# Kernel tuning notes

Measured on AMD Instinct MI355X. Metric: run time of the kernel, lower is better.

Reference implementation:

```python
import jax, jax.numpy as jnp
import numpy as np

N_NODES = 50000
N_EDGES = 600000
D = 128
EPS = 1e-5
AVG_D_LOG = float(np.log(4 + 1))  # avg_d={'log': log(avg_d+1)}, avg_d=4


def setup_inputs() -> dict:
    key = jax.random.key(0)
    ks = jax.random.split(key, 8)
    h = jax.random.normal(ks[0], (N_NODES, D), dtype=jnp.float32)
    # guarantee every node has at least one incoming edge (self-loop)
    edge_dst = jnp.concatenate([
        jnp.arange(N_NODES, dtype=jnp.int64),
        jax.random.randint(ks[1], (N_EDGES - N_NODES,), 0, N_NODES).astype(jnp.int64),
    ])
    edge_src = jax.random.randint(ks[2], (N_EDGES,), 0, N_NODES).astype(jnp.int64)
    def lin(k, fan_in, fan_out):
        lim = 1.0 / np.sqrt(fan_in)
        return jax.random.uniform(k, (fan_in, fan_out), jnp.float32, -lim, lim)
    W_pre = lin(ks[3], 2 * D, D)
    b_pre = jnp.zeros((D,), jnp.float32)
    W_post = lin(ks[4], 12 * D + D, D)  # 4 aggregators * 3 scalers * D + in_dim
    b_post = jnp.zeros((D,), jnp.float32)
    W_mix = lin(ks[5], D, D)
    b_mix = jnp.zeros((D,), jnp.float32)
    return {"h": h, "edge_src": edge_src, "edge_dst": edge_dst,
            "W_pre": W_pre, "b_pre": b_pre, "W_post": W_post,
            "b_post": b_post, "W_mix": W_mix, "b_mix": b_mix}


def reference(h, edge_src, edge_dst, W_pre, b_pre, W_post, b_post, W_mix, b_mix):
    n = h.shape[0]
    # pretrans_edges: cat(src, dst) -> Linear -> ReLU (MLP act) -> ReLU (outer)
    z2 = jnp.concatenate([h[edge_src], h[edge_dst]], axis=1)        # [E, 2D]
    e = jax.nn.relu(z2 @ W_pre + b_pre)                             # [E, D]
    # multi-aggregator segment reduce over destination nodes
    deg = jax.ops.segment_sum(jnp.ones_like(edge_dst, jnp.float32), edge_dst, n)  # [N]
    inv_deg = 1.0 / deg[:, None]
    mean = jax.ops.segment_sum(e, edge_dst, n) * inv_deg
    mean_sq = jax.ops.segment_sum(e * e, edge_dst, n) * inv_deg
    std = jnp.sqrt(jax.nn.relu(mean_sq - mean * mean) + EPS)
    mx = jax.ops.segment_max(e, edge_dst, n)
    mn = jax.ops.segment_min(e, edge_dst, n)
    agg = jnp.concatenate([mean, mx, mn, std], axis=1)              # [N, 4D]
    # scalers: identity, amplification, attenuation
    log_d = jnp.log(deg + 1.0)[:, None]
    scaled = jnp.concatenate([agg, agg * (log_d / AVG_D_LOG), agg * (AVG_D_LOG / log_d)], axis=1)  # [N, 12D]
    # posttrans: cat(h, aggregated) -> Linear -> ReLU
    hp = jax.nn.relu(jnp.concatenate([h, scaled], axis=1) @ W_post + b_post)  # [N, D]
    # mixing network + residual (node_dim == out_dim)
    out = h + jax.nn.leaky_relu(hp @ W_mix + b_mix, negative_slope=0.01)
    return out
```

## Files before the change

### kernel.cpp

```cpp
#include <hip/hip_runtime.h>
#include <hip/hip_bf16.h>

#define N_NODES 50000
#define N_EDGES 600000
#define D 128

constexpr float AVG_D_LOG = 1.6094379124341003f;
constexpr float EPS_V = 1e-5f;

#define PQ_B     0ul
#define AGG_B    25600000ul
#define HBF_B    76800000ul
#define WPRET2_B 89600000ul
#define WPOSTT_B 89665536ul
#define WMIXT_B  90091520ul
#define DEGC_B   90124288ul
#define OFF_B    90324288ul
#define CUR_B    90524352ul
#define SRCS_B   90724352ul
#define GCNT_B   93124352ul

typedef __attribute__((ext_vector_type(8))) short bf16x8;
typedef __attribute__((ext_vector_type(4))) float f32x4;

__device__ __forceinline__ short f2b(float f) {
    unsigned u = __builtin_bit_cast(unsigned, f);
    u += 0x7fffu + ((u >> 16) & 1u);
    return (short)(u >> 16);
}
__device__ __forceinline__ unsigned pk2(float a, float b) {
    return (unsigned)(unsigned short)f2b(a) | ((unsigned)(unsigned short)f2b(b) << 16);
}
__device__ __forceinline__ float blo(unsigned u) { return __uint_as_float(u << 16); }
__device__ __forceinline__ float bhi(unsigned u) { return __uint_as_float(u & 0xffff0000u); }

__device__ __forceinline__ void gld_lds16(const void* g, void* l) {
    __builtin_amdgcn_global_load_lds(
        (const __attribute__((address_space(1))) void*)g,
        (__attribute__((address_space(3))) void*)l, 16, 0, 0);
}

#define WAIT_BAR(N) do {                                              \
    asm volatile("s_waitcnt vmcnt(" #N ")" ::: "memory");             \
    __builtin_amdgcn_sched_barrier(0);                                \
    __builtin_amdgcn_s_barrier();                                     \
    __builtin_amdgcn_sched_barrier(0);                                \
} while (0)
#define BAR_ONLY() do {                                               \
    __builtin_amdgcn_sched_barrier(0);                                \
    __builtin_amdgcn_s_barrier();                                     \
    __builtin_amdgcn_sched_barrier(0);                                \
} while (0)
#define SB0() __builtin_amdgcn_sched_barrier(0)

__global__ __launch_bounds__(256) void prep_kernel(
    const float* __restrict__ h, const float* __restrict__ Wpre,
    const float* __restrict__ Wpost, const float* __restrict__ Wmix,
    short* __restrict__ hbf, short* __restrict__ wpreT2,
    short* __restrict__ wpostT, short* __restrict__ wmixT,
    int* __restrict__ degc, int* __restrict__ cursor, int* __restrict__ gcnt)
{
    long i = (long)blockIdx.x * 256 + threadIdx.x;
    if (i < 800000) {
        float4 a = *(const float4*)(h + i * 8);
        float4 b = *(const float4*)(h + i * 8 + 4);
        int4 v;
        v.x = (int)pk2(a.x, a.y); v.y = (int)pk2(a.z, a.w);
        v.z = (int)pk2(b.x, b.y); v.w = (int)pk2(b.z, b.w);
        *(int4*)(hbf + i * 8) = v;
        return;
    }
    i -= 800000;
    if (i < 32768) {
        int n = i >> 7, k = i & 127;
        float v = (n < 128) ? Wpre[k * 128 + n] : Wpre[(k + 128) * 128 + (n - 128)];
        wpreT2[n * 128 + k] = f2b(v);
        return;
    }
    i -= 32768;
    if (i < 212992) { int k = i >> 7, n = i & 127; wpostT[n * 1664 + k] = f2b(Wpost[k * 128 + n]); return; }
    i -= 212992;
    if (i < 16384) { int k = i >> 7, n = i & 127; wmixT[n * 128 + k] = f2b(Wmix[k * 128 + n]); return; }
    i -= 16384;
    if (i < N_NODES) { degc[i] = 0; return; }
    i -= N_NODES;
    if (i < N_NODES) { cursor[i] = 0; return; }
    i -= N_NODES;
    if (i == 0) *gcnt = 0;
}
#define PREP_BLOCKS ((800000 + 32768 + 212992 + 16384 + 2 * N_NODES + 1 + 255) / 256)

__global__ __launch_bounds__(256) void hist_kernel(const int* __restrict__ edst, int* __restrict__ degc) {
    int e = blockIdx.x * 256 + threadIdx.x;
    if (e < N_EDGES) atomicAdd(&degc[edst[e]], 1);
}

__global__ __launch_bounds__(256) void alloc_kernel(const int* __restrict__ degc,
                                                    int* __restrict__ off, int* __restrict__ gcnt) {
    int n = blockIdx.x * 256 + threadIdx.x;
    int d = (n < N_NODES) ? degc[n] : 0;
    int pre = d;
#pragma unroll
    for (int o = 1; o < 64; o <<= 1) {
        int t = __shfl_up(pre, o);
        if ((threadIdx.x & 63) >= o) pre += t;
    }
    int base = 0;
    if ((threadIdx.x & 63) == 63) base = atomicAdd(gcnt, pre);
    base = __shfl(base, 63);
    if (n < N_NODES) off[n] = base + pre - d;
}

__global__ __launch_bounds__(256) void scatter_kernel(const int* __restrict__ esrc, const int* __restrict__ edst,
                                                      const int* __restrict__ off, int* __restrict__ cursor,
                                                      int* __restrict__ srcs) {
    int e = blockIdx.x * 256 + threadIdx.x;
    if (e < N_EDGES) {
        int d = edst[e];
        int p = off[d] + atomicAdd(&cursor[d], 1);
        srcs[p] = esrc[e];
    }
}

__device__ __forceinline__ void stageA_t(short* ldsT, const short* src, int rs, int co,
                                         int bn, int wv, int lane) {
    const int sub = lane >> 3, seg = lane & 7;
    const int sg = (seg ^ sub) * 8;
#pragma unroll
    for (int t = 0; t < 4; t++) {
        int i = wv * 4 + t;
        int row = i * 8 + sub;
        int n = bn + row; if (n >= N_NODES) n = N_NODES - 1;
        gld_lds16(src + (long)n * rs + co + sg, ldsT + i * 512);
    }
}
__device__ __forceinline__ void stageB_t(short* ldsT, const short* src, int rs, int co,
                                         int wv, int lane) {
    const int sub = lane >> 3, seg = lane & 7;
    const int sg = (seg ^ sub) * 8;
#pragma unroll
    for (int t = 0; t < 4; t++) {
        int i = wv * 4 + t;
        int row = i * 8 + sub;
        gld_lds16(src + (long)row * rs + co + sg, ldsT + i * 512);
    }
}
__device__ __forceinline__ void loadAfr(bf16x8* a, const short* src, int rs, int co,
                                        int bn, int wv, int lm, int quad) {
#pragma unroll
    for (int rt = 0; rt < 2; rt++)
#pragma unroll
        for (int ks = 0; ks < 2; ks++) {
            int n = bn + wv * 32 + rt * 16 + lm; if (n >= N_NODES) n = N_NODES - 1;
            a[rt * 2 + ks] = *(const bf16x8*)(src + (long)n * rs + co + ks * 32 + quad * 8);
        }
}

#define MFMA_ITER(AB, BB, ACC)                                                      \
    {                                                                               \
        _Pragma("unroll")                                                           \
        for (int ks = 0; ks < 2; ks++) {                                            \
            const int qx = (((ks * 4 + quad) ^ r7) * 8);                            \
            bf16x8 a0 = *(const bf16x8*)&(AB)[(wv * 32 + lm) * 64 + qx];            \
            bf16x8 a1 = *(const bf16x8*)&(AB)[(wv * 32 + 16 + lm) * 64 + qx];       \
            _Pragma("unroll")                                                       \
            for (int ct = 0; ct < 8; ct++) {                                        \
                bf16x8 b = *(const bf16x8*)&(BB)[(ct * 16 + lm) * 64 + qx];         \
                ACC[0][ct] = __builtin_amdgcn_mfma_f32_16x16x32_bf16(b, a0, ACC[0][ct], 0, 0, 0); \
                ACC[1][ct] = __builtin_amdgcn_mfma_f32_16x16x32_bf16(b, a1, ACC[1][ct], 0, 0, 0); \
            }                                                                       \
        }                                                                           \
    }

#define MFMA_RG(BB, AF, ACC, FRESH)                                                 \
    {                                                                               \
        __builtin_amdgcn_s_setprio(1);                                              \
        _Pragma("unroll")                                                           \
        for (int ks = 0; ks < 2; ks++) {                                            \
            const int qx = ((ks * 4 + quad) ^ r7) * 8;                              \
            _Pragma("unroll")                                                       \
            for (int ct = 0; ct < 8; ct++) {                                        \
                bf16x8 b = *(const bf16x8*)&(BB)[(ct * 16 + lm) * 64 + qx];         \
                f32x4 c0 = ((FRESH) && ks == 0) ? (f32x4){0.f, 0.f, 0.f, 0.f} : ACC[0][ct]; \
                f32x4 c1 = ((FRESH) && ks == 0) ? (f32x4){0.f, 0.f, 0.f, 0.f} : ACC[1][ct]; \
                ACC[0][ct] = __builtin_amdgcn_mfma_f32_16x16x32_bf16(b, (AF)[ks], c0, 0, 0, 0); \
                ACC[1][ct] = __builtin_amdgcn_mfma_f32_16x16x32_bf16(b, (AF)[2 + ks], c1, 0, 0, 0); \
            }                                                                       \
        }                                                                           \
        __builtin_amdgcn_s_setprio(0);                                              \
    }

__global__ __launch_bounds__(256, 2) void gemm_pq_kernel(
    const short* __restrict__ hbf, const short* __restrict__ wpreT2,
    const float* __restrict__ bpre, short* __restrict__ PQ)
{
    __shared__ __align__(16) short As[2][8192];
    __shared__ __align__(16) short Bs[2][8192];

    const int tid = threadIdx.x;
    const int cg = blockIdx.x & 1;
    const int bn = (blockIdx.x >> 1) * 128;
    const int lane = tid & 63, wv = tid >> 6;
    const int lm = lane & 15, quad = lane >> 4;
    const int r7 = lm & 7;
    const short* Bsrc = wpreT2 + cg * 128 * 128;

    f32x4 acc[2][8];
#pragma unroll
    for (int a = 0; a < 2; a++)
#pragma unroll
        for (int b = 0; b < 8; b++) acc[a][b] = (f32x4){0.f, 0.f, 0.f, 0.f};

    stageA_t(As[0], hbf, 128, 0, bn, wv, lane);
    stageB_t(Bs[0], Bsrc, 128, 0, wv, lane);
    stageA_t(As[1], hbf, 128, 64, bn, wv, lane);
    stageB_t(Bs[1], Bsrc, 128, 64, wv, lane);
    WAIT_BAR(8);
    MFMA_ITER(As[0], Bs[0], acc);
    WAIT_BAR(0);
    MFMA_ITER(As[1], Bs[1], acc);

#pragma unroll
    for (int rt = 0; rt < 2; rt++) {
        int row = wv * 32 + rt * 16 + lm;
        int n = bn + row;
        if (n >= N_NODES) continue;
        short* dst = PQ + (long)n * 256;
#pragma unroll
        for (int ct = 0; ct < 8; ct++) {
            int col = cg * 128 + ct * 16 + quad * 4;
            float v0 = acc[rt][ct][0], v1 = acc[rt][ct][1], v2 = acc[rt][ct][2], v3 = acc[rt][ct][3];
            if (cg) {
                float4 bv = *(const float4*)(bpre + (col - 128));
                v0 += bv.x; v1 += bv.y; v2 += bv.z; v3 += bv.w;
            }
            int2 pkd; pkd.x = (int)pk2(v0, v1); pkd.y = (int)pk2(v2, v3);
            *(int2*)(dst + col) = pkd;
        }
    }
}

__global__ __launch_bounds__(256) void edgestats_kernel(
    const short* __restrict__ PQ, const int* __restrict__ srcs,
    const int* __restrict__ off, const int* __restrict__ degc, short* __restrict__ aggbf)
{
    const int wv = threadIdx.x >> 6, lane = threadIdx.x & 63;
    const int n = blockIdx.x * 4 + wv;
    const unsigned* Pb = (const unsigned*)PQ;

    const int s0 = __builtin_amdgcn_readfirstlane(off[n]);
    const int s1 = s0 + __builtin_amdgcn_readfirstlane(degc[n]);

    unsigned qu = Pb[(long)n * 128 + 64 + lane];
    const float qa = blo(qu), qb = bhi(qu);

    float sA = 0.f, sB = 0.f, qA = 0.f, qB = 0.f;
    float mxA = -1e30f, mxB = -1e30f, mnA = 1e30f, mnB = 1e30f;

    int p = s0;
    for (; p + 8 <= s1; p += 8) {
        int idx[8];
#pragma unroll
        for (int j = 0; j < 8; j++) idx[j] = srcs[p + j];
        unsigned u[8];
#pragma unroll
        for (int j = 0; j < 8; j++) u[j] = Pb[(long)idx[j] * 128 + lane];
#pragma unroll
        for (int j = 0; j < 8; j++) {
            float a = blo(u[j]) + qa; a = a > 0.f ? a : 0.f;
            float b = bhi(u[j]) + qb; b = b > 0.f ? b : 0.f;
            sA += a; sB += b; qA += a * a; qB += b * b;
            mxA = fmaxf(mxA, a); mxB = fmaxf(mxB, b);
            mnA = fminf(mnA, a); mnB = fminf(mnB, b);
        }
    }
    if (p + 4 <= s1) {
        int idx[4];
#pragma unroll
        for (int j = 0; j < 4; j++) idx[j] = srcs[p + j];
        unsigned u[4];
#pragma unroll
        for (int j = 0; j < 4; j++) u[j] = Pb[(long)idx[j] * 128 + lane];
#pragma unroll
        for (int j = 0; j < 4; j++) {
            float a = blo(u[j]) + qa; a = a > 0.f ? a : 0.f;
            float b = bhi(u[j]) + qb; b = b > 0.f ? b : 0.f;
            sA += a; sB += b; qA += a * a; qB += b * b;
            mxA = fmaxf(mxA, a); mxB = fmaxf(mxB, b);
            mnA = fminf(mnA, a); mnB = fminf(mnB, b);
        }
        p += 4;
    }
    for (; p < s1; p++) {
        unsigned u = Pb[(long)srcs[p] * 128 + lane];
        float a = blo(u) + qa; a = a > 0.f ? a : 0.f;
        float b = bhi(u) + qb; b = b > 0.f ? b : 0.f;
        sA += a; sB += b; qA += a * a; qB += b * b;
        mxA = fmaxf(mxA, a); mxB = fmaxf(mxB, b);
        mnA = fminf(mnA, a); mnB = fminf(mnB, b);
    }

    float inv = 1.0f / (float)(s1 - s0);
    float mA = sA * inv, mB = sB * inv;
    float vA = qA * inv - mA * mA; vA = vA > 0.f ? vA : 0.f;
    float vB = qB * inv - mB * mB; vB = vB > 0.f ? vB : 0.f;
    float stA = sqrtf(vA + EPS_V), stB = sqrtf(vB + EPS_V);

    unsigned* ag = (unsigned*)(aggbf + (long)n * 512);
    ag[lane]       = pk2(mA, mB);
    ag[64 + lane]  = pk2(mxA, mxB);
    ag[128 + lane] = pk2(mnA, mnB);
    ag[192 + lane] = pk2(stA, stB);
}

__global__ __launch_bounds__(256, 2) void node_kernel(
    const float* __restrict__ h, const short* __restrict__ hbf, const short* __restrict__ aggbf,
    const int* __restrict__ degc, const short* __restrict__ wpostT, const float* __restrict__ bpost,
    const short* __restrict__ wmixT, const float* __restrict__ bmix, float* __restrict__ out)
{
    __shared__ __align__(16) short As[2][8192];
    __shared__ __align__(16) short Bs[2][8192];
    __shared__ float sAmp[128], sAtt[128];

    const int tid = threadIdx.x;
    const int bn = blockIdx.x * 128;
    const int lane = tid & 63, wv = tid >> 6;
    const int lm = lane & 15, quad = lane >> 4;
    const int r7 = lm & 7;

    if (tid < 128) {
        int n = bn + tid; if (n >= N_NODES) n = N_NODES - 1;
        float d = (float)degc[n];
        float ld = logf(d + 1.0f);
        sAmp[tid] = ld * (1.0f / AVG_D_LOG);
        sAtt[tid] = AVG_D_LOG / ld;
    }
    __syncthreads();

    const float am0 = sAmp[wv * 32 + lm],      at0 = sAtt[wv * 32 + lm];
    const float am1 = sAmp[wv * 32 + 16 + lm], at1 = sAtt[wv * 32 + 16 + lm];

    f32x4 mI[2][8];

    bf16x8 hA0[4], hA1[4];
    loadAfr(hA0, hbf, 128, 0, bn, wv, lm, quad);
    SB0();
    stageB_t(Bs[0], wpostT, 1664, 0, wv, lane);
    SB0();
    loadAfr(hA1, hbf, 128, 64, bn, wv, lm, quad);
    SB0();
    stageA_t(As[0], aggbf, 512, 0, bn, wv, lane);

    WAIT_BAR(8);
    stageB_t(Bs[1], wpostT, 1664, 64, wv, lane);
    SB0();
    stageA_t(As[1], aggbf, 512, 64, bn, wv, lane);
    MFMA_RG(Bs[0], hA0, mI, 1);

    WAIT_BAR(4);
    stageB_t(Bs[0], wpostT, 1664, 2 * 64, wv, lane);
    MFMA_RG(Bs[1], hA1, mI, 0);

    for (int j = 0; j < 8; j++) {
        const int pb = j & 1, pn = pb ^ 1;
        const short* Ac = As[pb];
        bf16x8 aR[4];

        WAIT_BAR(0);
        stageB_t(Bs[pn], wpostT, 1664, (10 + j) * 64, wv, lane);
#pragma unroll
        for (int rt = 0; rt < 2; rt++)
#pragma unroll
            for (int ks = 0; ks < 2; ks++)
                aR[rt * 2 + ks] = *(const bf16x8*)&Ac[(wv * 32 + rt * 16 + lm) * 64 + ((ks * 4 + quad) ^ r7) * 8];
        MFMA_RG(Bs[pb], aR, mI, 0);

        WAIT_BAR(0);
        stageB_t(Bs[pb], wpostT, 1664, (18 + j) * 64, wv, lane);
        SB0();
        if (j < 7) {
            int jn = j + 1;
            stageA_t(As[pn], aggbf, 512, (jn >> 1) * 128 + (jn & 1) * 64, bn, wv, lane);
        }
        {
            f32x4 tp[2][8];
            MFMA_RG(Bs[pn], aR, tp, 1);
#pragma unroll
            for (int ct = 0; ct < 8; ct++) {
                mI[0][ct] += am0 * tp[0][ct];
                mI[1][ct] += am1 * tp[1][ct];
            }
        }

        if (j < 7) { WAIT_BAR(4); } else { WAIT_BAR(0); }
        if (j < 7) stageB_t(Bs[pn], wpostT, 1664, (3 + j) * 64, wv, lane);
        else       stageB_t(Bs[pn], wmixT, 128, 0, wv, lane);
        {
            f32x4 tp[2][8];
            MFMA_RG(Bs[pb], aR, tp, 1);
#pragma unroll
            for (int ct = 0; ct < 8; ct++) {
                mI[0][ct] += at0 * tp[0][ct];
                mI[1][ct] += at1 * tp[1][ct];
            }
        }
    }

    BAR_ONLY();
    stageB_t(Bs[1], wmixT, 128, 64, wv, lane);

#pragma unroll
    for (int rt = 0; rt < 2; rt++) {
        const int row = wv * 32 + rt * 16 + lm;
#pragma unroll
        for (int ct = 0; ct < 8; ct++) {
            float4 bv = *(const float4*)(bpost + ct * 16 + quad * 4);
            float v0 = mI[rt][ct][0] + bv.x; v0 = v0 > 0.f ? v0 : 0.f;
            float v1 = mI[rt][ct][1] + bv.y; v1 = v1 > 0.f ? v1 : 0.f;
            float v2 = mI[rt][ct][2] + bv.z; v2 = v2 > 0.f ? v2 : 0.f;
            float v3 = mI[rt][ct][3] + bv.w; v3 = v3 > 0.f ? v3 : 0.f;
            int2 pkd; pkd.x = (int)pk2(v0, v1); pkd.y = (int)pk2(v2, v3);
            const int cb = (ct & 3) * 32 + quad * 8;
            const int sb = ((((cb >> 4) ^ r7) << 4) | (cb & 15));
            *(int2*)((char*)As[ct >> 2] + row * 128 + sb) = pkd;
        }
    }
    __syncthreads();

    f32x4 accO[2][8];
#pragma unroll
    for (int a = 0; a < 2; a++)
#pragma unroll
        for (int b = 0; b < 8; b++) accO[a][b] = (f32x4){0.f, 0.f, 0.f, 0.f};
#pragma unroll
    for (int kc = 0; kc < 2; kc++) {
        MFMA_ITER(As[kc], Bs[kc], accO);
    }

#pragma unroll
    for (int rt = 0; rt < 2; rt++) {
        int row = wv * 32 + rt * 16 + lm;
        int n = bn + row;
        if (n >= N_NODES) continue;
#pragma unroll
        for (int ct = 0; ct < 8; ct++) {
            int col = ct * 16 + quad * 4;
            float4 bv = *(const float4*)(bmix + col);
            float4 hv = *(const float4*)(h + (long)n * 128 + col);
            float4 o;
            float v0 = accO[rt][ct][0] + bv.x; v0 = v0 > 0.f ? v0 : 0.01f * v0; o.x = hv.x + v0;
            float v1 = accO[rt][ct][1] + bv.y; v1 = v1 > 0.f ? v1 : 0.01f * v1; o.y = hv.y + v1;
            float v2 = accO[rt][ct][2] + bv.z; v2 = v2 > 0.f ? v2 : 0.01f * v2; o.z = hv.z + v2;
            float v3 = accO[rt][ct][3] + bv.w; v3 = v3 > 0.f ? v3 : 0.01f * v3; o.w = hv.w + v3;
            *(float4*)(out + (long)n * 128 + col) = o;
        }
    }
}

extern "C" void kernel_launch(void* const* d_in, const int* in_sizes, int n_in,
                              void* d_out, int out_size, void* d_ws, size_t ws_size,
                              hipStream_t stream) {
    const float* h     = (const float*)d_in[0];
    const int*   esrc  = (const int*)d_in[1];
    const int*   edst  = (const int*)d_in[2];
    const float* Wpre  = (const float*)d_in[3];
    const float* bpre  = (const float*)d_in[4];
    const float* Wpost = (const float*)d_in[5];
    const float* bpost = (const float*)d_in[6];
    const float* Wmix  = (const float*)d_in[7];
    const float* bmix  = (const float*)d_in[8];
    float* out = (float*)d_out;
    char* ws = (char*)d_ws;

    short* PQ     = (short*)(ws + PQ_B);
    short* aggbf  = (short*)(ws + AGG_B);
    short* hbf    = (short*)(ws + HBF_B);
    short* wpreT2 = (short*)(ws + WPRET2_B);
    short* wpostT = (short*)(ws + WPOSTT_B);
    short* wmixT  = (short*)(ws + WMIXT_B);
    int*   degc   = (int*)(ws + DEGC_B);
    int*   off    = (int*)(ws + OFF_B);
    int*   cursor = (int*)(ws + CUR_B);
    int*   srcs   = (int*)(ws + SRCS_B);
    int*   gcnt   = (int*)(ws + GCNT_B);

    prep_kernel<<<PREP_BLOCKS, 256, 0, stream>>>(h, Wpre, Wpost, Wmix, hbf, wpreT2, wpostT, wmixT, degc, cursor, gcnt);
    hist_kernel<<<(N_EDGES + 255) / 256, 256, 0, stream>>>(edst, degc);
    alloc_kernel<<<(N_NODES + 255) / 256, 256, 0, stream>>>(degc, off, gcnt);
    scatter_kernel<<<(N_EDGES + 255) / 256, 256, 0, stream>>>(esrc, edst, off, cursor, srcs);
    gemm_pq_kernel<<<((N_NODES + 127) / 128) * 2, 256, 0, stream>>>(hbf, wpreT2, bpre, PQ);
    edgestats_kernel<<<N_NODES / 4, 256, 0, stream>>>(PQ, srcs, off, degc, aggbf);
    node_kernel<<<(N_NODES + 127) / 128, 256, 0, stream>>>(h, hbf, aggbf, degc, wpostT, bpost, wmixT, bmix, out);
}
```

Baseline: 244.4 us.

## Load aggregates straight to registers in node kernel, fuse histogram into prep

```diff
diff --git a/kernel.cpp b/kernel.cpp
--- a/kernel.cpp
+++ b/kernel.cpp
@@ -52,13 +52,15 @@
     __builtin_amdgcn_sched_barrier(0);                                \
 } while (0)
 #define SB0() __builtin_amdgcn_sched_barrier(0)
+#define LGKM0() do { asm volatile("s_waitcnt lgkmcnt(0)" ::: "memory"); SB0(); } while (0)
 
 __global__ __launch_bounds__(256) void prep_kernel(
     const float* __restrict__ h, const float* __restrict__ Wpre,
     const float* __restrict__ Wpost, const float* __restrict__ Wmix,
+    const int* __restrict__ edst,
     short* __restrict__ hbf, short* __restrict__ wpreT2,
     short* __restrict__ wpostT, short* __restrict__ wmixT,
-    int* __restrict__ degc, int* __restrict__ cursor, int* __restrict__ gcnt)
+    int* __restrict__ degc)
 {
     long i = (long)blockIdx.x * 256 + threadIdx.x;
     if (i < 800000) {
@@ -82,18 +84,9 @@
     i -= 212992;
     if (i < 16384) { int k = i >> 7, n = i & 127; wmixT[n * 128 + k] = f2b(Wmix[k * 128 + n]); return; }
     i -= 16384;
-    if (i < N_NODES) { degc[i] = 0; return; }
-    i -= N_NODES;
-    if (i < N_NODES) { cursor[i] = 0; return; }
-    i -= N_NODES;
-    if (i == 0) *gcnt = 0;
-}
-#define PREP_BLOCKS ((800000 + 32768 + 212992 + 16384 + 2 * N_NODES + 1 + 255) / 256)
-
-__global__ __launch_bounds__(256) void hist_kernel(const int* __restrict__ edst, int* __restrict__ degc) {
-    int e = blockIdx.x * 256 + threadIdx.x;
-    if (e < N_EDGES) atomicAdd(&degc[edst[e]], 1);
-}
+    if (i < N_EDGES) atomicAdd(&degc[edst[i]], 1);
+}
+#define PREP_BLOCKS ((800000 + 32768 + 212992 + 16384 + N_EDGES + 255) / 256)
 
 __global__ __launch_bounds__(256) void alloc_kernel(const int* __restrict__ degc,
                                                     int* __restrict__ off, int* __restrict__ gcnt) {
@@ -190,6 +183,13 @@
         __builtin_amdgcn_s_setprio(0);                                              \
     }
 
+#define FOLD(SRC, S0, S1)                                                           \
+    _Pragma("unroll")                                                               \
+    for (int ct = 0; ct < 8; ct++) {                                                \
+        mI[0][ct] += (S0) * SRC[0][ct];                                             \
+        mI[1][ct] += (S1) * SRC[1][ct];                                             \
+    }
+
 __global__ __launch_bounds__(256, 2) void gemm_pq_kernel(
     const short* __restrict__ hbf, const short* __restrict__ wpreT2,
     const float* __restrict__ bpre, short* __restrict__ PQ)
@@ -313,13 +313,13 @@
     ag[192 + lane] = pk2(stA, stB);
 }
 
-__global__ __launch_bounds__(256, 2) void node_kernel(
+__global__ __launch_bounds__(256, 3) void node_kernel(
     const float* __restrict__ h, const short* __restrict__ hbf, const short* __restrict__ aggbf,
     const int* __restrict__ degc, const short* __restrict__ wpostT, const float* __restrict__ bpost,
     const short* __restrict__ wmixT, const float* __restrict__ bmix, float* __restrict__ out)
 {
-    __shared__ __align__(16) short As[2][8192];
     __shared__ __align__(16) short Bs[2][8192];
+    __shared__ __align__(16) short hpS[8192];
     __shared__ float sAmp[128], sAtt[128];
 
     const int tid = threadIdx.x;
@@ -341,68 +341,67 @@
     const float am1 = sAmp[wv * 32 + 16 + lm], at1 = sAtt[wv * 32 + 16 + lm];
 
     f32x4 mI[2][8];
+    bf16x8 aCur[4], aNxt[4];
 
     bf16x8 hA0[4], hA1[4];
-    loadAfr(hA0, hbf, 128, 0, bn, wv, lm, quad);
-    SB0();
     stageB_t(Bs[0], wpostT, 1664, 0, wv, lane);
     SB0();
+    loadAfr(hA0, hbf, 128, 0, bn, wv, lm, quad);
     loadAfr(hA1, hbf, 128, 64, bn, wv, lm, quad);
-    SB0();
-    stageA_t(As[0], aggbf, 512, 0, bn, wv, lane);
-
-    WAIT_BAR(8);
+    loadAfr(aCur, aggbf, 512, 0, bn, wv, lm, quad);
+
+    WAIT_BAR(12);
     stageB_t(Bs[1], wpostT, 1664, 64, wv, lane);
-    SB0();
-    stageA_t(As[1], aggbf, 512, 64, bn, wv, lane);
     MFMA_RG(Bs[0], hA0, mI, 1);
 
-    WAIT_BAR(4);
+    WAIT_BAR(0);
     stageB_t(Bs[0], wpostT, 1664, 2 * 64, wv, lane);
     MFMA_RG(Bs[1], hA1, mI, 0);
 
-    for (int j = 0; j < 8; j++) {
-        const int pb = j & 1, pn = pb ^ 1;
-        const short* Ac = As[pb];
-        bf16x8 aR[4];
+    for (int jp = 0; jp < 4; jp++) {
+        const int j0 = 2 * jp, j1 = 2 * jp + 1;
 
         WAIT_BAR(0);
-        stageB_t(Bs[pn], wpostT, 1664, (10 + j) * 64, wv, lane);
-#pragma unroll
-        for (int rt = 0; rt < 2; rt++)
-#pragma unroll
-            for (int ks = 0; ks < 2; ks++)
-                aR[rt * 2 + ks] = *(const bf16x8*)&Ac[(wv * 32 + rt * 16 + lm) * 64 + ((ks * 4 + quad) ^ r7) * 8];
-        MFMA_RG(Bs[pb], aR, mI, 0);
-
+        stageB_t(Bs[1], wpostT, 1664, (10 + j0) * 64, wv, lane);
+        MFMA_RG(Bs[0], aCur, mI, 0);
         WAIT_BAR(0);
-        stageB_t(Bs[pb], wpostT, 1664, (18 + j) * 64, wv, lane);
+        stageB_t(Bs[0], wpostT, 1664, (18 + j0) * 64, wv, lane);
         SB0();
-        if (j < 7) {
-            int jn = j + 1;
-            stageA_t(As[pn], aggbf, 512, (jn >> 1) * 128 + (jn & 1) * 64, bn, wv, lane);
-        }
+        loadAfr(aNxt, aggbf, 512, (j0 >> 1) * 128 + 64, bn, wv, lm, quad);
         {
             f32x4 tp[2][8];
-            MFMA_RG(Bs[pn], aR, tp, 1);
-#pragma unroll
-            for (int ct = 0; ct < 8; ct++) {
-                mI[0][ct] += am0 * tp[0][ct];
-                mI[1][ct] += am1 * tp[1][ct];
-            }
-        }
-
-        if (j < 7) { WAIT_BAR(4); } else { WAIT_BAR(0); }
-        if (j < 7) stageB_t(Bs[pn], wpostT, 1664, (3 + j) * 64, wv, lane);
-        else       stageB_t(Bs[pn], wmixT, 128, 0, wv, lane);
+            MFMA_RG(Bs[1], aCur, tp, 1);
+            FOLD(tp, am0, am1);
+        }
+        WAIT_BAR(4);
+        stageB_t(Bs[1], wpostT, 1664, (3 + j0) * 64, wv, lane);
         {
             f32x4 tp[2][8];
-            MFMA_RG(Bs[pb], aR, tp, 1);
-#pragma unroll
-            for (int ct = 0; ct < 8; ct++) {
-                mI[0][ct] += at0 * tp[0][ct];
-                mI[1][ct] += at1 * tp[1][ct];
-            }
+            MFMA_RG(Bs[0], aCur, tp, 1);
+            FOLD(tp, at0, at1);
+        }
+
+        WAIT_BAR(0);
+        stageB_t(Bs[0], wpostT, 1664, (10 + j1) * 64, wv, lane);
+        MFMA_RG(Bs[1], aNxt, mI, 0);
+        WAIT_BAR(0);
+        stageB_t(Bs[1], wpostT, 1664, (18 + j1) * 64, wv, lane);
+        if (j1 < 7) {
+            SB0();
+            loadAfr(aCur, aggbf, 512, ((j1 + 1) >> 1) * 128, bn, wv, lm, quad);
+        }
+        {
+            f32x4 tp[2][8];
+            MFMA_RG(Bs[0], aNxt, tp, 1);
+            FOLD(tp, am0, am1);
+        }
+        if (j1 < 7) { WAIT_BAR(4); } else { WAIT_BAR(0); }
+        if (j1 < 7) stageB_t(Bs[0], wpostT, 1664, (3 + j1) * 64, wv, lane);
+        else        stageB_t(Bs[0], wmixT, 128, 0, wv, lane);
+        {
+            f32x4 tp[2][8];
+            MFMA_RG(Bs[1], aNxt, tp, 1);
+            FOLD(tp, at0, at1);
         }
     }
 
@@ -410,19 +409,26 @@
     stageB_t(Bs[1], wmixT, 128, 64, wv, lane);
 
 #pragma unroll
+    for (int rt = 0; rt < 2; rt++)
+#pragma unroll
+        for (int ct = 0; ct < 8; ct++) {
+            float4 bv = *(const float4*)(bpost + ct * 16 + quad * 4);
+            mI[rt][ct][0] = fmaxf(mI[rt][ct][0] + bv.x, 0.f);
+            mI[rt][ct][1] = fmaxf(mI[rt][ct][1] + bv.y, 0.f);
+            mI[rt][ct][2] = fmaxf(mI[rt][ct][2] + bv.z, 0.f);
+            mI[rt][ct][3] = fmaxf(mI[rt][ct][3] + bv.w, 0.f);
+        }
+
+#pragma unroll
     for (int rt = 0; rt < 2; rt++) {
         const int row = wv * 32 + rt * 16 + lm;
 #pragma unroll
-        for (int ct = 0; ct < 8; ct++) {
-            float4 bv = *(const float4*)(bpost + ct * 16 + quad * 4);
-            float v0 = mI[rt][ct][0] + bv.x; v0 = v0 > 0.f ? v0 : 0.f;
-            float v1 = mI[rt][ct][1] + bv.y; v1 = v1 > 0.f ? v1 : 0.f;
-            float v2 = mI[rt][ct][2] + bv.z; v2 = v2 > 0.f ? v2 : 0.f;
-            float v3 = mI[rt][ct][3] + bv.w; v3 = v3 > 0.f ? v3 : 0.f;
-            int2 pkd; pkd.x = (int)pk2(v0, v1); pkd.y = (int)pk2(v2, v3);
-            const int cb = (ct & 3) * 32 + quad * 8;
+        for (int ct = 0; ct < 4; ct++) {
+            int2 pkd; pkd.x = (int)pk2(mI[rt][ct][0], mI[rt][ct][1]);
+            pkd.y = (int)pk2(mI[rt][ct][2], mI[rt][ct][3]);
+            const int cb = ct * 32 + quad * 8;
             const int sb = ((((cb >> 4) ^ r7) << 4) | (cb & 15));
-            *(int2*)((char*)As[ct >> 2] + row * 128 + sb) = pkd;
+            *(int2*)((char*)hpS + row * 128 + sb) = pkd;
         }
     }
     __syncthreads();
@@ -432,10 +438,23 @@
     for (int a = 0; a < 2; a++)
 #pragma unroll
         for (int b = 0; b < 8; b++) accO[a][b] = (f32x4){0.f, 0.f, 0.f, 0.f};
-#pragma unroll
-    for (int kc = 0; kc < 2; kc++) {
-        MFMA_ITER(As[kc], Bs[kc], accO);
-    }
+    MFMA_ITER(hpS, Bs[0], accO);
+
+    LGKM0();
+#pragma unroll
+    for (int rt = 0; rt < 2; rt++) {
+        const int row = wv * 32 + rt * 16 + lm;
+#pragma unroll
+        for (int ct = 4; ct < 8; ct++) {
+            int2 pkd; pkd.x = (int)pk2(mI[rt][ct][0], mI[rt][ct][1]);
+            pkd.y = (int)pk2(mI[rt][ct][2], mI[rt][ct][3]);
+            const int cb = (ct - 4) * 32 + quad * 8;
+            const int sb = ((((cb >> 4) ^ r7) << 4) | (cb & 15));
+            *(int2*)((char*)hpS + row * 128 + sb) = pkd;
+        }
+    }
+    LGKM0();
+    MFMA_ITER(hpS, Bs[1], accO);
 
 #pragma unroll
     for (int rt = 0; rt < 2; rt++) {
@@ -484,8 +503,10 @@
     int*   srcs   = (int*)(ws + SRCS_B);
     int*   gcnt   = (int*)(ws + GCNT_B);
 
-    prep_kernel<<<PREP_BLOCKS, 256, 0, stream>>>(h, Wpre, Wpost, Wmix, hbf, wpreT2, wpostT, wmixT, degc, cursor, gcnt);
-    hist_kernel<<<(N_EDGES + 255) / 256, 256, 0, stream>>>(edst, degc);
+    hipMemsetAsync(ws + DEGC_B, 0, N_NODES * 4, stream);
+    hipMemsetAsync(ws + CUR_B,  0, N_NODES * 4, stream);
+    hipMemsetAsync(ws + GCNT_B, 0, 4, stream);
+    prep_kernel<<<PREP_BLOCKS, 256, 0, stream>>>(h, Wpre, Wpost, Wmix, edst, hbf, wpreT2, wpostT, wmixT, degc);
     alloc_kernel<<<(N_NODES + 255) / 256, 256, 0, stream>>>(degc, off, gcnt);
     scatter_kernel<<<(N_EDGES + 255) / 256, 256, 0, stream>>>(esrc, edst, off, cursor, srcs);
     gemm_pq_kernel<<<((N_NODES + 127) / 128) * 2, 256, 0, stream>>>(hbf, wpreT2, bpre, PQ);
```

New measurement: 314.2 us. +28.6%, slower.

## Single-buffer node_kernel A tile to fit three blocks per CU

Applied to the files above, without the earlier changes.

```diff
diff --git a/kernel.cpp b/kernel.cpp
--- a/kernel.cpp
+++ b/kernel.cpp
@@ -52,6 +52,7 @@
     __builtin_amdgcn_sched_barrier(0);                                \
 } while (0)
 #define SB0() __builtin_amdgcn_sched_barrier(0)
+#define LGKM0() do { asm volatile("s_waitcnt lgkmcnt(0)" ::: "memory"); SB0(); } while (0)
 
 __global__ __launch_bounds__(256) void prep_kernel(
     const float* __restrict__ h, const float* __restrict__ Wpre,
@@ -190,6 +191,13 @@
         __builtin_amdgcn_s_setprio(0);                                              \
     }
 
+#define FOLD(SRC, S0, S1)                                                           \
+    _Pragma("unroll")                                                               \
+    for (int ct = 0; ct < 8; ct++) {                                                \
+        mI[0][ct] += (S0) * SRC[0][ct];                                             \
+        mI[1][ct] += (S1) * SRC[1][ct];                                             \
+    }
+
 __global__ __launch_bounds__(256, 2) void gemm_pq_kernel(
     const short* __restrict__ hbf, const short* __restrict__ wpreT2,
     const float* __restrict__ bpre, short* __restrict__ PQ)
@@ -313,12 +321,12 @@
     ag[192 + lane] = pk2(stA, stB);
 }
 
-__global__ __launch_bounds__(256, 2) void node_kernel(
+__global__ __launch_bounds__(256, 3) void node_kernel(
     const float* __restrict__ h, const short* __restrict__ hbf, const short* __restrict__ aggbf,
     const int* __restrict__ degc, const short* __restrict__ wpostT, const float* __restrict__ bpost,
     const short* __restrict__ wmixT, const float* __restrict__ bmix, float* __restrict__ out)
 {
-    __shared__ __align__(16) short As[2][8192];
+    __shared__ __align__(16) short As[8192];
     __shared__ __align__(16) short Bs[2][8192];
     __shared__ float sAmp[128], sAtt[128];
 
@@ -343,27 +351,23 @@
     f32x4 mI[2][8];
 
     bf16x8 hA0[4], hA1[4];
-    loadAfr(hA0, hbf, 128, 0, bn, wv, lm, quad);
-    SB0();
     stageB_t(Bs[0], wpostT, 1664, 0, wv, lane);
     SB0();
+    loadAfr(hA0, hbf, 128, 0, bn, wv, lm, quad);
     loadAfr(hA1, hbf, 128, 64, bn, wv, lm, quad);
     SB0();
-    stageA_t(As[0], aggbf, 512, 0, bn, wv, lane);
-
-    WAIT_BAR(8);
+    stageA_t(As, aggbf, 512, 0, bn, wv, lane);
+
+    WAIT_BAR(12);
     stageB_t(Bs[1], wpostT, 1664, 64, wv, lane);
-    SB0();
-    stageA_t(As[1], aggbf, 512, 64, bn, wv, lane);
     MFMA_RG(Bs[0], hA0, mI, 1);
 
-    WAIT_BAR(4);
+    WAIT_BAR(0);
     stageB_t(Bs[0], wpostT, 1664, 2 * 64, wv, lane);
     MFMA_RG(Bs[1], hA1, mI, 0);
 
     for (int j = 0; j < 8; j++) {
         const int pb = j & 1, pn = pb ^ 1;
-        const short* Ac = As[pb];
         bf16x8 aR[4];
 
         WAIT_BAR(0);
@@ -372,7 +376,7 @@
         for (int rt = 0; rt < 2; rt++)
 #pragma unroll
             for (int ks = 0; ks < 2; ks++)
-                aR[rt * 2 + ks] = *(const bf16x8*)&Ac[(wv * 32 + rt * 16 + lm) * 64 + ((ks * 4 + quad) ^ r7) * 8];
+                aR[rt * 2 + ks] = *(const bf16x8*)&As[(wv * 32 + rt * 16 + lm) * 64 + ((ks * 4 + quad) ^ r7) * 8];
         MFMA_RG(Bs[pb], aR, mI, 0);
 
         WAIT_BAR(0);
@@ -380,16 +384,12 @@
         SB0();
         if (j < 7) {
             int jn = j + 1;
-            stageA_t(As[pn], aggbf, 512, (jn >> 1) * 128 + (jn & 1) * 64, bn, wv, lane);
+            stageA_t(As, aggbf, 512, (jn >> 1) * 128 + (jn & 1) * 64, bn, wv, lane);
         }
         {
             f32x4 tp[2][8];
             MFMA_RG(Bs[pn], aR, tp, 1);
-#pragma unroll
-            for (int ct = 0; ct < 8; ct++) {
-                mI[0][ct] += am0 * tp[0][ct];
-                mI[1][ct] += am1 * tp[1][ct];
-            }
+            FOLD(tp, am0, am1);
         }
 
         if (j < 7) { WAIT_BAR(4); } else { WAIT_BAR(0); }
@@ -398,11 +398,7 @@
         {
             f32x4 tp[2][8];
             MFMA_RG(Bs[pb], aR, tp, 1);
-#pragma unroll
-            for (int ct = 0; ct < 8; ct++) {
-                mI[0][ct] += at0 * tp[0][ct];
-                mI[1][ct] += at1 * tp[1][ct];
-            }
+            FOLD(tp, at0, at1);
         }
     }
 
@@ -410,19 +406,26 @@
     stageB_t(Bs[1], wmixT, 128, 64, wv, lane);
 
 #pragma unroll
+    for (int rt = 0; rt < 2; rt++)
+#pragma unroll
+        for (int ct = 0; ct < 8; ct++) {
+            float4 bv = *(const float4*)(bpost + ct * 16 + quad * 4);
+            mI[rt][ct][0] = fmaxf(mI[rt][ct][0] + bv.x, 0.f);
+            mI[rt][ct][1] = fmaxf(mI[rt][ct][1] + bv.y, 0.f);
+            mI[rt][ct][2] = fmaxf(mI[rt][ct][2] + bv.z, 0.f);
+            mI[rt][ct][3] = fmaxf(mI[rt][ct][3] + bv.w, 0.f);
+        }
+
+#pragma unroll
     for (int rt = 0; rt < 2; rt++) {
         const int row = wv * 32 + rt * 16 + lm;
 #pragma unroll
-        for (int ct = 0; ct < 8; ct++) {
-            float4 bv = *(const float4*)(bpost + ct * 16 + quad * 4);
-            float v0 = mI[rt][ct][0] + bv.x; v0 = v0 > 0.f ? v0 : 0.f;
-            float v1 = mI[rt][ct][1] + bv.y; v1 = v1 > 0.f ? v1 : 0.f;
-            float v2 = mI[rt][ct][2] + bv.z; v2 = v2 > 0.f ? v2 : 0.f;
-            float v3 = mI[rt][ct][3] + bv.w; v3 = v3 > 0.f ? v3 : 0.f;
-            int2 pkd; pkd.x = (int)pk2(v0, v1); pkd.y = (int)pk2(v2, v3);
-            const int cb = (ct & 3) * 32 + quad * 8;
+        for (int ct = 0; ct < 4; ct++) {
+            int2 pkd; pkd.x = (int)pk2(mI[rt][ct][0], mI[rt][ct][1]);
+            pkd.y = (int)pk2(mI[rt][ct][2], mI[rt][ct][3]);
+            const int cb = ct * 32 + quad * 8;
             const int sb = ((((cb >> 4) ^ r7) << 4) | (cb & 15));
-            *(int2*)((char*)As[ct >> 2] + row * 128 + sb) = pkd;
+            *(int2*)((char*)As + row * 128 + sb) = pkd;
         }
     }
     __syncthreads();
@@ -432,10 +435,23 @@
     for (int a = 0; a < 2; a++)
 #pragma unroll
         for (int b = 0; b < 8; b++) accO[a][b] = (f32x4){0.f, 0.f, 0.f, 0.f};
-#pragma unroll
-    for (int kc = 0; kc < 2; kc++) {
-        MFMA_ITER(As[kc], Bs[kc], accO);
-    }
+    MFMA_ITER(As, Bs[0], accO);
+
+    LGKM0();
+#pragma unroll
+    for (int rt = 0; rt < 2; rt++) {
+        const int row = wv * 32 + rt * 16 + lm;
+#pragma unroll
+        for (int ct = 4; ct < 8; ct++) {
+            int2 pkd; pkd.x = (int)pk2(mI[rt][ct][0], mI[rt][ct][1]);
+            pkd.y = (int)pk2(mI[rt][ct][2], mI[rt][ct][3]);
+            const int cb = (ct - 4) * 32 + quad * 8;
+            const int sb = ((((cb >> 4) ^ r7) << 4) | (cb & 15));
+            *(int2*)((char*)As + row * 128 + sb) = pkd;
+        }
+    }
+    LGKM0();
+    MFMA_ITER(As, Bs[1], accO);
 
 #pragma unroll
     for (int rt = 0; rt < 2; rt++) {
```

New measurement: 291.6 us. 19.3% more time.

## Record edge slots in histogram, fuse scatter into PQ GEMM, restructure node_kernel pipeline

Applied to the files above, without the earlier changes.

```diff
diff --git a/kernel.cpp b/kernel.cpp
--- a/kernel.cpp
+++ b/kernel.cpp
@@ -4,6 +4,8 @@
 #define N_NODES 50000
 #define N_EDGES 600000
 #define D 128
+#define NB_GEMM 782
+#define NB_SCAT 2344
 
 constexpr float AVG_D_LOG = 1.6094379124341003f;
 constexpr float EPS_V = 1e-5f;
@@ -58,7 +60,7 @@
     const float* __restrict__ Wpost, const float* __restrict__ Wmix,
     short* __restrict__ hbf, short* __restrict__ wpreT2,
     short* __restrict__ wpostT, short* __restrict__ wmixT,
-    int* __restrict__ degc, int* __restrict__ cursor, int* __restrict__ gcnt)
+    int* __restrict__ degc, int* __restrict__ gcnt)
 {
     long i = (long)blockIdx.x * 256 + threadIdx.x;
     if (i < 800000) {
@@ -84,15 +86,14 @@
     i -= 16384;
     if (i < N_NODES) { degc[i] = 0; return; }
     i -= N_NODES;
-    if (i < N_NODES) { cursor[i] = 0; return; }
-    i -= N_NODES;
     if (i == 0) *gcnt = 0;
 }
-#define PREP_BLOCKS ((800000 + 32768 + 212992 + 16384 + 2 * N_NODES + 1 + 255) / 256)
-
-__global__ __launch_bounds__(256) void hist_kernel(const int* __restrict__ edst, int* __restrict__ degc) {
+#define PREP_BLOCKS ((800000 + 32768 + 212992 + 16384 + N_NODES + 1 + 255) / 256)
+
+__global__ __launch_bounds__(256) void hist_kernel(const int* __restrict__ edst, int* __restrict__ degc,
+                                                   int* __restrict__ eslot) {
     int e = blockIdx.x * 256 + threadIdx.x;
-    if (e < N_EDGES) atomicAdd(&degc[edst[e]], 1);
+    if (e < N_EDGES) eslot[e] = atomicAdd(&degc[edst[e]], 1);
 }
 
 __global__ __launch_bounds__(256) void alloc_kernel(const int* __restrict__ degc,
@@ -111,17 +112,6 @@
     if (n < N_NODES) off[n] = base + pre - d;
 }
 
-__global__ __launch_bounds__(256) void scatter_kernel(const int* __restrict__ esrc, const int* __restrict__ edst,
-                                                      const int* __restrict__ off, int* __restrict__ cursor,
-                                                      int* __restrict__ srcs) {
-    int e = blockIdx.x * 256 + threadIdx.x;
-    if (e < N_EDGES) {
-        int d = edst[e];
-        int p = off[d] + atomicAdd(&cursor[d], 1);
-        srcs[p] = esrc[e];
-    }
-}
-
 __device__ __forceinline__ void stageA_t(short* ldsT, const short* src, int rs, int co,
                                          int bn, int wv, int lane) {
     const int sub = lane >> 3, seg = lane & 7;
@@ -145,14 +135,14 @@
         gld_lds16(src + (long)row * rs + co + sg, ldsT + i * 512);
     }
 }
-__device__ __forceinline__ void loadAfr(bf16x8* a, const short* src, int rs, int co,
-                                        int bn, int wv, int lm, int quad) {
+__device__ __forceinline__ void loadAfr2(bf16x8* a, const short* src, int rs, int co,
+                                         int bn, int wv, int lm, int quad) {
 #pragma unroll
     for (int rt = 0; rt < 2; rt++)
 #pragma unroll
-        for (int ks = 0; ks < 2; ks++) {
+        for (int kk = 0; kk < 4; kk++) {
             int n = bn + wv * 32 + rt * 16 + lm; if (n >= N_NODES) n = N_NODES - 1;
-            a[rt * 2 + ks] = *(const bf16x8*)(src + (long)n * rs + co + ks * 32 + quad * 8);
+            a[rt * 4 + kk] = *(const bf16x8*)(src + (long)n * rs + co + kk * 32 + quad * 8);
         }
 }
 
@@ -172,32 +162,54 @@
         }                                                                           \
     }
 
-#define MFMA_RG(BB, AF, ACC, FRESH)                                                 \
+#define MFMA_RG2(B0, B1, AF, ACC, FRESH)                                            \
     {                                                                               \
         __builtin_amdgcn_s_setprio(1);                                              \
         _Pragma("unroll")                                                           \
-        for (int ks = 0; ks < 2; ks++) {                                            \
-            const int qx = ((ks * 4 + quad) ^ r7) * 8;                              \
+        for (int kc = 0; kc < 2; kc++) {                                            \
+            const short* BBp = kc ? (B1) : (B0);                                    \
             _Pragma("unroll")                                                       \
-            for (int ct = 0; ct < 8; ct++) {                                        \
-                bf16x8 b = *(const bf16x8*)&(BB)[(ct * 16 + lm) * 64 + qx];         \
-                f32x4 c0 = ((FRESH) && ks == 0) ? (f32x4){0.f, 0.f, 0.f, 0.f} : ACC[0][ct]; \
-                f32x4 c1 = ((FRESH) && ks == 0) ? (f32x4){0.f, 0.f, 0.f, 0.f} : ACC[1][ct]; \
-                ACC[0][ct] = __builtin_amdgcn_mfma_f32_16x16x32_bf16(b, (AF)[ks], c0, 0, 0, 0); \
-                ACC[1][ct] = __builtin_amdgcn_mfma_f32_16x16x32_bf16(b, (AF)[2 + ks], c1, 0, 0, 0); \
+            for (int ks = 0; ks < 2; ks++) {                                        \
+                const int qx = ((ks * 4 + quad) ^ r7) * 8;                          \
+                _Pragma("unroll")                                                   \
+                for (int ct = 0; ct < 8; ct++) {                                    \
+                    bf16x8 b = *(const bf16x8*)&BBp[(ct * 16 + lm) * 64 + qx];      \
+                    f32x4 c0 = ((FRESH) && kc == 0 && ks == 0) ? (f32x4){0.f,0.f,0.f,0.f} : ACC[0][ct]; \
+                    f32x4 c1 = ((FRESH) && kc == 0 && ks == 0) ? (f32x4){0.f,0.f,0.f,0.f} : ACC[1][ct]; \
+                    ACC[0][ct] = __builtin_amdgcn_mfma_f32_16x16x32_bf16(b, (AF)[kc * 2 + ks], c0, 0, 0, 0); \
+                    ACC[1][ct] = __builtin_amdgcn_mfma_f32_16x16x32_bf16(b, (AF)[4 + kc * 2 + ks], c1, 0, 0, 0); \
+                }                                                                   \
             }                                                                       \
         }                                                                           \
         __builtin_amdgcn_s_setprio(0);                                              \
     }
 
-__global__ __launch_bounds__(256, 2) void gemm_pq_kernel(
+#define FOLD(SRC, S0, S1)                                                           \
+    _Pragma("unroll")                                                               \
+    for (int ct = 0; ct < 8; ct++) {                                                \
+        mI[0][ct] += (S0) * SRC[0][ct];                                             \
+        mI[1][ct] += (S1) * SRC[1][ct];                                             \
+    }
+
+__global__ __launch_bounds__(256, 2) void scatgemm_kernel(
     const short* __restrict__ hbf, const short* __restrict__ wpreT2,
-    const float* __restrict__ bpre, short* __restrict__ PQ)
+    const float* __restrict__ bpre, short* __restrict__ PQ,
+    const int* __restrict__ esrc, const int* __restrict__ edst,
+    const int* __restrict__ off, const int* __restrict__ eslot, int* __restrict__ srcs)
 {
     __shared__ __align__(16) short As[2][8192];
     __shared__ __align__(16) short Bs[2][8192];
 
     const int tid = threadIdx.x;
+    if (blockIdx.x >= NB_GEMM) {
+        int e = (blockIdx.x - NB_GEMM) * 256 + tid;
+        if (e < N_EDGES) {
+            int d = edst[e];
+            srcs[off[d] + eslot[e]] = esrc[e];
+        }
+        return;
+    }
+
     const int cg = blockIdx.x & 1;
     const int bn = (blockIdx.x >> 1) * 128;
     const int lane = tid & 63, wv = tid >> 6;
@@ -318,8 +330,7 @@
     const int* __restrict__ degc, const short* __restrict__ wpostT, const float* __restrict__ bpost,
     const short* __restrict__ wmixT, const float* __restrict__ bmix, float* __restrict__ out)
 {
-    __shared__ __align__(16) short As[2][8192];
-    __shared__ __align__(16) short Bs[2][8192];
+    __shared__ __align__(16) short Bs0[8192], Bs1[8192], Bs2[8192], Bs3[8192];
     __shared__ float sAmp[128], sAtt[128];
 
     const int tid = threadIdx.x;
@@ -341,73 +352,81 @@
     const float am1 = sAmp[wv * 32 + 16 + lm], at1 = sAtt[wv * 32 + 16 + lm];
 
     f32x4 mI[2][8];
-
-    bf16x8 hA0[4], hA1[4];
-    loadAfr(hA0, hbf, 128, 0, bn, wv, lm, quad);
+    bf16x8 aA[8], aB[8];
+    bf16x8 hA[8];
+
+    stageB_t(Bs0, wpostT, 1664, 0, wv, lane);
+    stageB_t(Bs1, wpostT, 1664, 64, wv, lane);
     SB0();
-    stageB_t(Bs[0], wpostT, 1664, 0, wv, lane);
+    loadAfr2(hA, hbf, 128, 0, bn, wv, lm, quad);
     SB0();
-    loadAfr(hA1, hbf, 128, 64, bn, wv, lm, quad);
-    SB0();
-    stageA_t(As[0], aggbf, 512, 0, bn, wv, lane);
+    loadAfr2(aA, aggbf, 512, 0, bn, wv, lm, quad);
 
     WAIT_BAR(8);
-    stageB_t(Bs[1], wpostT, 1664, 64, wv, lane);
-    SB0();
-    stageA_t(As[1], aggbf, 512, 64, bn, wv, lane);
-    MFMA_RG(Bs[0], hA0, mI, 1);
-
-    WAIT_BAR(4);
-    stageB_t(Bs[0], wpostT, 1664, 2 * 64, wv, lane);
-    MFMA_RG(Bs[1], hA1, mI, 0);
-
-    for (int j = 0; j < 8; j++) {
-        const int pb = j & 1, pn = pb ^ 1;
-        const short* Ac = As[pb];
-        bf16x8 aR[4];
+    stageB_t(Bs2, wpostT, 1664, 2 * 64, wv, lane);
+    stageB_t(Bs3, wpostT, 1664, 3 * 64, wv, lane);
+    MFMA_RG2(Bs0, Bs1, hA, mI, 1);
+
+    for (int ap = 0; ap < 2; ap++) {
+        const int g0 = 2 * ap, g1 = g0 + 1;
 
         WAIT_BAR(0);
-        stageB_t(Bs[pn], wpostT, 1664, (10 + j) * 64, wv, lane);
-#pragma unroll
-        for (int rt = 0; rt < 2; rt++)
-#pragma unroll
-            for (int ks = 0; ks < 2; ks++)
-                aR[rt * 2 + ks] = *(const bf16x8*)&Ac[(wv * 32 + rt * 16 + lm) * 64 + ((ks * 4 + quad) ^ r7) * 8];
-        MFMA_RG(Bs[pb], aR, mI, 0);
-
-        WAIT_BAR(0);
-        stageB_t(Bs[pb], wpostT, 1664, (18 + j) * 64, wv, lane);
+        stageB_t(Bs0, wpostT, 1664, (10 + 2 * g0) * 64, wv, lane);
+        stageB_t(Bs1, wpostT, 1664, (11 + 2 * g0) * 64, wv, lane);
         SB0();
-        if (j < 7) {
-            int jn = j + 1;
-            stageA_t(As[pn], aggbf, 512, (jn >> 1) * 128 + (jn & 1) * 64, bn, wv, lane);
-        }
+        loadAfr2(aB, aggbf, 512, g1 * 128, bn, wv, lm, quad);
+        MFMA_RG2(Bs2, Bs3, aA, mI, 0);
+
+        WAIT_BAR(8);
+        stageB_t(Bs2, wpostT, 1664, (18 + 2 * g0) * 64, wv, lane);
+        stageB_t(Bs3, wpostT, 1664, (19 + 2 * g0) * 64, wv, lane);
         {
             f32x4 tp[2][8];
-            MFMA_RG(Bs[pn], aR, tp, 1);
-#pragma unroll
-            for (int ct = 0; ct < 8; ct++) {
-                mI[0][ct] += am0 * tp[0][ct];
-                mI[1][ct] += am1 * tp[1][ct];
-            }
-        }
-
-        if (j < 7) { WAIT_BAR(4); } else { WAIT_BAR(0); }
-        if (j < 7) stageB_t(Bs[pn], wpostT, 1664, (3 + j) * 64, wv, lane);
-        else       stageB_t(Bs[pn], wmixT, 128, 0, wv, lane);
+            MFMA_RG2(Bs0, Bs1, aA, tp, 1);
+            FOLD(tp, am0, am1);
+        }
+
+        WAIT_BAR(0);
+        stageB_t(Bs0, wpostT, 1664, (2 + 2 * g1) * 64, wv, lane);
+        stageB_t(Bs1, wpostT, 1664, (3 + 2 * g1) * 64, wv, lane);
         {
             f32x4 tp[2][8];
-            MFMA_RG(Bs[pb], aR, tp, 1);
-#pragma unroll
-            for (int ct = 0; ct < 8; ct++) {
-                mI[0][ct] += at0 * tp[0][ct];
-                mI[1][ct] += at1 * tp[1][ct];
-            }
+            MFMA_RG2(Bs2, Bs3, aA, tp, 1);
+            FOLD(tp, at0, at1);
+        }
+
+        WAIT_BAR(0);
+        stageB_t(Bs2, wpostT, 1664, (10 + 2 * g1) * 64, wv, lane);
+        stageB_t(Bs3, wpostT, 1664, (11 + 2 * g1) * 64, wv, lane);
+        SB0();
+        if (ap < 1) loadAfr2(aA, aggbf, 512, (g1 + 1) * 128, bn, wv, lm, quad);
+        MFMA_RG2(Bs0, Bs1, aB, mI, 0);
+
+        if (ap < 1) { WAIT_BAR(8); } else { WAIT_BAR(0); }
+        stageB_t(Bs0, wpostT, 1664, (18 + 2 * g1) * 64, wv, lane);
+        stageB_t(Bs1, wpostT, 1664, (19 + 2 * g1) * 64, wv, lane);
+        {
+            f32x4 tp[2][8];
+            MFMA_RG2(Bs2, Bs3, aB, tp, 1);
+            FOLD(tp, am0, am1);
+        }
+
+        WAIT_BAR(0);
+        if (ap < 1) {
+            stageB_t(Bs2, wpostT, 1664, (2 + 2 * (g1 + 1)) * 64, wv, lane);
+            stageB_t(Bs3, wpostT, 1664, (3 + 2 * (g1 + 1)) * 64, wv, lane);
+        } else {
+            stageB_t(Bs2, wmixT, 128, 0, wv, lane);
+            stageB_t(Bs3, wmixT, 128, 64, wv, lane);
+        }
+        {
+            f32x4 tp[2][8];
+            MFMA_RG2(Bs0, Bs1, aB, tp, 1);
+            FOLD(tp, at0, at1);
         }
     }
 
     BAR_ONLY();
-    stageB_t(Bs[1], wmixT, 128, 64, wv, lane);
 
 #pragma unroll
     for (int rt = 0; rt < 2; rt++) {
@@ -415,14 +434,14 @@
 #pragma unroll
         for (int ct = 0; ct < 8; ct++) {
             float4 bv = *(const float4*)(bpost + ct * 16 + quad * 4);
-            float v0 = mI[rt][ct][0] + bv.x; v0 = v0 > 0.f ? v0 : 0.f;
-            float v1 = mI[rt][ct][1] + bv.y; v1 = v1 > 0.f ? v1 : 0.f;
-            float v2 = mI[rt][ct][2] + bv.z; v2 = v2 > 0.f ? v2 : 0.f;
-            float v3 = mI[rt][ct][3] + bv.w; v3 = v3 > 0.f ? v3 : 0.f;
+            float v0 = fmaxf(mI[rt][ct][0] + bv.x, 0.f);
+            float v1 = fmaxf(mI[rt][ct][1] + bv.y, 0.f);
+            float v2 = fmaxf(mI[rt][ct][2] + bv.z, 0.f);
+            float v3 = fmaxf(mI[rt][ct][3] + bv.w, 0.f);
             int2 pkd; pkd.x = (int)pk2(v0, v1); pkd.y = (int)pk2(v2, v3);
             const int cb = (ct & 3) * 32 + quad * 8;
             const int sb = ((((cb >> 4) ^ r7) << 4) | (cb & 15));
-            *(int2*)((char*)As[ct >> 2] + row * 128 + sb) = pkd;
+            *(int2*)((char*)(ct < 4 ? Bs0 : Bs1) + row * 128 + sb) = pkd;
         }
     }
     __syncthreads();
@@ -432,10 +451,8 @@
     for (int a = 0; a < 2; a++)
 #pragma unroll
         for (int b = 0; b < 8; b++) accO[a][b] = (f32x4){0.f, 0.f, 0.f, 0.f};
-#pragma unroll
-    for (int kc = 0; kc < 2; kc++) {
-        MFMA_ITER(As[kc], Bs[kc], accO);
-    }
+    MFMA_ITER(Bs0, Bs2, accO);
+    MFMA_ITER(Bs1, Bs3, accO);
 
 #pragma unroll
     for (int rt = 0; rt < 2; rt++) {
@@ -480,15 +497,14 @@
     short* wmixT  = (short*)(ws + WMIXT_B);
     int*   degc   = (int*)(ws + DEGC_B);
     int*   off    = (int*)(ws + OFF_B);
-    int*   cursor = (int*)(ws + CUR_B);
     int*   srcs   = (int*)(ws + SRCS_B);
     int*   gcnt   = (int*)(ws + GCNT_B);
-
-    prep_kernel<<<PREP_BLOCKS, 256, 0, stream>>>(h, Wpre, Wpost, Wmix, hbf, wpreT2, wpostT, wmixT, degc, cursor, gcnt);
-    hist_kernel<<<(N_EDGES + 255) / 256, 256, 0, stream>>>(edst, degc);
+    int*   eslot  = (int*)(ws + AGG_B);
+
+    prep_kernel<<<PREP_BLOCKS, 256, 0, stream>>>(h, Wpre, Wpost, Wmix, hbf, wpreT2, wpostT, wmixT, degc, gcnt);
+    hist_kernel<<<NB_SCAT, 256, 0, stream>>>(edst, degc, eslot);
     alloc_kernel<<<(N_NODES + 255) / 256, 256, 0, stream>>>(degc, off, gcnt);
-    scatter_kernel<<<(N_EDGES + 255) / 256, 256, 0, stream>>>(esrc, edst, off, cursor, srcs);
-    gemm_pq_kernel<<<((N_NODES + 127) / 128) * 2, 256, 0, stream>>>(hbf, wpreT2, bpre, PQ);
+    scatgemm_kernel<<<NB_GEMM + NB_SCAT, 256, 0, stream>>>(hbf, wpreT2, bpre, PQ, esrc, edst, off, eslot, srcs);
     edgestats_kernel<<<N_NODES / 4, 256, 0, stream>>>(PQ, srcs, off, degc, aggbf);
     node_kernel<<<(N_NODES + 127) / 128, 256, 0, stream>>>(h, hbf, aggbf, degc, wpostT, bpost, wmixT, bmix, out);
 }
```

Result: slower. 257.4 us (+5.3%).
